# Performance work log

Hardware: AMD Instinct MI355X
Metric: run time of the kernel (lower is better)

## Reference

```python
import jax, jax.numpy as jnp
import numpy as np

N_NODES = 100000


def sage_conv(x, src, dst, Wl, bl, Wr):
    # PyG SAGEConv (aggr='mean'): out = lin_l(mean_{j in N(i)} x_j) + lin_r(x_i)
    msg = x[src]                                                   # [E, d] gather
    agg = jax.ops.segment_sum(msg, dst, num_segments=N_NODES)      # [N, d]
    cnt = jax.ops.segment_sum(jnp.ones((src.shape[0], 1), x.dtype), dst,
                              num_segments=N_NODES)                # [N, 1]
    mean = agg / jnp.maximum(cnt, 1.0)
    return mean @ Wl + bl + x @ Wr


def setup_inputs() -> dict:
    key = jax.random.key(0)
    ks = jax.random.split(key, 9)
    N, E, D_IN = N_NODES, 3200000, 64
    x = jax.random.normal(ks[0], (N, D_IN), dtype=jnp.float32)
    edge_index = jax.random.randint(ks[1], (2, E), 0, N, dtype=jnp.int64)

    def glorot(k, fan_in, fan_out):
        lim = float(np.sqrt(6.0 / (fan_in + fan_out)))
        return jax.random.uniform(k, (fan_in, fan_out), jnp.float32, -lim, lim)

    return {
        "x": x,
        "edge_index": edge_index,
        "W1l": glorot(ks[2], D_IN, 64), "b1": jnp.zeros((64,), jnp.float32),
        "W1r": glorot(ks[3], D_IN, 64),
        "W2l": glorot(ks[4], 64, 32), "b2": jnp.zeros((32,), jnp.float32),
        "W2r": glorot(ks[5], 64, 32),
        "W3l": glorot(ks[6], 32, 1), "b3": jnp.zeros((1,), jnp.float32),
        "W3r": glorot(ks[7], 32, 1),
    }


def reference(x, edge_index, W1l, b1, W1r, W2l, b2, W2r, W3l, b3, W3r):
    src, dst = edge_index[0], edge_index[1]
    h = jax.nn.relu(sage_conv(x, src, dst, W1l, b1, W1r))   # dropout: eval mode (identity)
    h = jax.nn.relu(sage_conv(h, src, dst, W2l, b2, W2r))
    h = sage_conv(h, src, dst, W3l, b3, W3r)
    return jax.nn.sigmoid(h)                                # [N, 1]
```

## Files before the change

kernel.cpp:

```cpp
#include <hip/hip_runtime.h>
#include <math.h>

#define NN 100000
#define NB 391
#define BT 8192
#define CAP 12288

typedef float vfloat2 __attribute__((ext_vector_type(2)));
typedef short short8 __attribute__((ext_vector_type(8)));
typedef float floatx4 __attribute__((ext_vector_type(4)));

__device__ __forceinline__ unsigned short f2bf(float f) {
    unsigned int u = __float_as_uint(f);
    u += 0x7fffu + ((u >> 16) & 1u);
    return (unsigned short)(u >> 16);
}

__device__ __forceinline__ unsigned char f2fp8(float f) {
    const int p = __builtin_amdgcn_cvt_pk_fp8_f32(f, f, 0, false);
    return (unsigned char)(p & 0xFF);
}
template <bool HI>
__device__ __forceinline__ vfloat2 fp8pk2(unsigned int w) {
    return __builtin_amdgcn_cvt_pk_f32_fp8((int)w, HI);
}

template <int D_IN, int CL, int CR, int NPB, int FUSE_IN>
__global__ void __launch_bounds__(256)
mlp_mfma_kernel(const float* __restrict__ in0,
                const float* __restrict__ in1,
                const float* __restrict__ Wl,
                const float* __restrict__ Wr,
                const float* __restrict__ bias,
                unsigned char* __restrict__ yout,
                float* __restrict__ zout,
                int n_nodes) {
    constexpr int COLS = CL + CR;
    constexpr int CT = COLS / 16;
    constexpr int KT = D_IN / 32;
    constexpr int NT = NPB / 16;
    constexpr int KG = D_IN / 8;
    __shared__ short sA[NT * KT * 64 * 8];
    __shared__ short sB[CT * KT * 64 * 8];
    __shared__ float sBias[CR];
    const int t = threadIdx.x;
    const int node0 = blockIdx.x * NPB;

    for (int i = t; i < NPB * KG; i += 256) {
        const int nl = i / KG, kg = i % KG;
        const int n = node0 + nl;
        float v[8];
        if (n < n_nodes) {
            const float4* p = (const float4*)(in0 + (long long)n * D_IN + kg * 8);
            float4 a0 = p[0], a1 = p[1];
            if (FUSE_IN) {
                const float4* q = (const float4*)(in1 + (long long)n * D_IN + kg * 8);
                const float4 b0 = q[0], b1 = q[1];
                a0.x = fmaxf(a0.x + b0.x, 0.f); a0.y = fmaxf(a0.y + b0.y, 0.f);
                a0.z = fmaxf(a0.z + b0.z, 0.f); a0.w = fmaxf(a0.w + b0.w, 0.f);
                a1.x = fmaxf(a1.x + b1.x, 0.f); a1.y = fmaxf(a1.y + b1.y, 0.f);
                a1.z = fmaxf(a1.z + b1.z, 0.f); a1.w = fmaxf(a1.w + b1.w, 0.f);
            }
            v[0] = a0.x; v[1] = a0.y; v[2] = a0.z; v[3] = a0.w;
            v[4] = a1.x; v[5] = a1.y; v[6] = a1.z; v[7] = a1.w;
        } else {
#pragma unroll
            for (int j = 0; j < 8; ++j) v[j] = 0.f;
        }
        short8 s;
#pragma unroll
        for (int j = 0; j < 8; ++j) s[j] = (short)f2bf(v[j]);
        const int nt = nl >> 4, m = nl & 15, kt = kg >> 2, quad = kg & 3;
        ((short8*)sA)[(nt * KT + kt) * 64 + quad * 16 + m] = s;
    }
    for (int i = t; i < CT * KT * 64; i += 256) {
        const int ct = i / (KT * 64);
        const int rem = i % (KT * 64);
        const int kt = rem / 64, L = rem % 64;
        const int c = ct * 16 + (L & 15);
        const int k0 = kt * 32 + (L >> 4) * 8;
        short8 s;
#pragma unroll
        for (int j = 0; j < 8; ++j) {
            const int k = k0 + j;
            const float w = (c < CL) ? Wl[k * CL + c] : Wr[k * CR + (c - CL)];
            s[j] = (short)f2bf(w);
        }
        ((short8*)sB)[i] = s;
    }
    for (int i = t; i < CR; i += 256) sBias[i] = bias[i];
    __syncthreads();

    const int w = t >> 6, lane = t & 63;
    short8 Bf[CT][KT];
#pragma unroll
    for (int ct = 0; ct < CT; ++ct)
#pragma unroll
        for (int kt = 0; kt < KT; ++kt)
            Bf[ct][kt] = ((short8*)sB)[(ct * KT + kt) * 64 + lane];
    const int col = lane & 15, quad = lane >> 4;
#pragma unroll
    for (int nti = 0; nti < NT / 4; ++nti) {
        const int nt = w * (NT / 4) + nti;
        short8 A[KT];
#pragma unroll
        for (int kt = 0; kt < KT; ++kt)
            A[kt] = ((short8*)sA)[(nt * KT + kt) * 64 + lane];
        const int nodeb = node0 + nt * 16 + quad * 4;
#pragma unroll
        for (int ct = 0; ct < CT; ++ct) {
            floatx4 acc = {0.f, 0.f, 0.f, 0.f};
#pragma unroll
            for (int kt = 0; kt < KT; ++kt)
                acc = __builtin_amdgcn_mfma_f32_16x16x32_bf16(A[kt], Bf[ct][kt], acc, 0, 0, 0);
            const int gc = ct * 16 + col;
#pragma unroll
            for (int r = 0; r < 4; ++r) {
                const int node = nodeb + r;
                if (node < n_nodes) {
                    if (gc < CL) {
                        constexpr int CH = CL / 2;
                        const int h = gc / CH;
                        yout[(size_t)h * n_nodes * CH +
                             (long long)node * CH + (gc & (CH - 1))] = f2fp8(acc[r]);
                    } else {
                        zout[(long long)node * CR + (gc - CL)] = acc[r] + sBias[gc - CL];
                    }
                }
            }
        }
    }
}

template <int D_IN>
__global__ void __launch_bounds__(256)
mlp3_kernel(const float* __restrict__ mean,
            const float* __restrict__ z,
            const float* __restrict__ W3l,
            const float* __restrict__ W3r,
            const float* __restrict__ b3,
            float* __restrict__ y,
            float* __restrict__ z3, int n_nodes) {
    __shared__ float swl[D_IN], swr[D_IN];
    const int t = threadIdx.x;
    if (t < D_IN) { swl[t] = W3l[t]; swr[t] = W3r[t]; }
    __syncthreads();
    const int n = blockIdx.x * 256 + t;
    if (n >= n_nodes) return;
    const float4* pm = (const float4*)(mean + (long long)n * D_IN);
    const float4* pz = (const float4*)(z + (long long)n * D_IN);
    float accl = 0.f, accr = 0.f;
#pragma unroll
    for (int q = 0; q < D_IN / 4; ++q) {
        const float4 m4 = pm[q];
        const float4 z4 = pz[q];
        const float h0 = fmaxf(m4.x + z4.x, 0.f);
        const float h1 = fmaxf(m4.y + z4.y, 0.f);
        const float h2 = fmaxf(m4.z + z4.z, 0.f);
        const float h3 = fmaxf(m4.w + z4.w, 0.f);
        accl += h0 * swl[4 * q] + h1 * swl[4 * q + 1] + h2 * swl[4 * q + 2] + h3 * swl[4 * q + 3];
        accr += h0 * swr[4 * q] + h1 * swr[4 * q + 1] + h2 * swr[4 * q + 2] + h3 * swr[4 * q + 3];
    }
    y[n] = accl;
    z3[n] = accr + b3[0];
}

__global__ void bucket_hist_kernel(const int* __restrict__ dst,
                                   int* __restrict__ bcnt, int n_edges) {
    __shared__ int lh[NB];
    for (int i = threadIdx.x; i < NB; i += 256) lh[i] = 0;
    __syncthreads();
    const int stride = gridDim.x * 256;
    for (int i = blockIdx.x * 256 + threadIdx.x; i < n_edges; i += stride)
        atomicAdd(&lh[dst[i] >> 8], 1);
    __syncthreads();
    for (int i = threadIdx.x; i < NB; i += 256)
        if (lh[i]) atomicAdd(&bcnt[i], lh[i]);
}

__global__ void __launch_bounds__(512)
bucket_scan_kernel(const int* __restrict__ bcnt, int* __restrict__ boffs,
                   int* __restrict__ bcursor) {
    __shared__ int s[512];
    const int t = threadIdx.x;
    const int v = (t < NB) ? bcnt[t] : 0;
    s[t] = v;
    __syncthreads();
    for (int off = 1; off < 512; off <<= 1) {
        const int tmp = (t >= off) ? s[t - off] : 0;
        __syncthreads();
        s[t] += tmp;
        __syncthreads();
    }
    const int excl = s[t] - v;
    if (t <= NB) boffs[t] = excl;
    if (t < NB) bcursor[t] = excl;
}

__global__ void __launch_bounds__(512)
bin_edges_kernel(const int* __restrict__ src, const int* __restrict__ dst,
                 int* __restrict__ bcursor, unsigned int* __restrict__ binned,
                 int n_edges) {
    __shared__ unsigned int stage[BT];
    __shared__ unsigned short sbkt[BT];
    __shared__ int lhist[512], lscan[512], lstart[512], gbase[512], lcur[512];
    const int t = threadIdx.x;
    const int e0 = blockIdx.x * BT;
    const int count = min(BT, n_edges - e0);
    lhist[t] = 0;
    __syncthreads();
    for (int i = t; i < count; i += 512) atomicAdd(&lhist[dst[e0 + i] >> 8], 1);
    __syncthreads();
    const int v = lhist[t];
    lscan[t] = v;
    __syncthreads();
    for (int off = 1; off < 512; off <<= 1) {
        const int tmp = (t >= off) ? lscan[t - off] : 0;
        __syncthreads();
        lscan[t] += tmp;
        __syncthreads();
    }
    const int excl = lscan[t] - v;
    lstart[t] = excl;
    lcur[t] = excl;
    if (t < NB && v > 0) gbase[t] = atomicAdd(&bcursor[t], v);
    __syncthreads();
    for (int i = t; i < count; i += 512) {
        const int d = dst[e0 + i];
        const int b = d >> 8;
        const int p = atomicAdd(&lcur[b], 1);
        stage[p] = (unsigned int)src[e0 + i] | ((unsigned int)(d & 255) << 17);
        sbkt[p] = (unsigned short)b;
    }
    __syncthreads();
    for (int i = t; i < count; i += 512) {
        const int b = sbkt[i];
        binned[gbase[b] + (i - lstart[b])] = stage[i];
    }
}

__global__ void __launch_bounds__(1024)
csr_sort_kernel(const unsigned int* __restrict__ binned,
                const int* __restrict__ boffs,
                int* __restrict__ ssrc, int* __restrict__ row_ptr,
                float* __restrict__ inv_deg, int n_nodes, int n_edges) {
    __shared__ int stage[CAP];
    __shared__ int hist[256];
    __shared__ int lexcl[256];
    __shared__ int lcur[256];
    const int t = threadIdx.x;
    const int b = blockIdx.x;
    const int s0 = boffs[b], s1 = boffs[b + 1];
    const int count = s1 - s0;
    if (t < 256) hist[t] = 0;
    __syncthreads();
    for (int i = t; i < count; i += 1024)
        atomicAdd(&hist[binned[s0 + i] >> 17], 1);
    __syncthreads();
    if (t < 256) lexcl[t] = hist[t];
    __syncthreads();
    for (int off = 1; off < 256; off <<= 1) {
        int tmp = 0;
        if (t < 256 && t >= off) tmp = lexcl[t - off];
        __syncthreads();
        if (t < 256) lexcl[t] += tmp;
        __syncthreads();
    }
    if (t < 256) {
        const int excl = lexcl[t] - hist[t];
        lcur[t] = excl;
        const int n = (b << 8) + t;
        if (n < n_nodes) {
            row_ptr[n] = s0 + excl;
            inv_deg[n] = 1.0f / (float)max(hist[t], 1);
        }
    }
    if (b == NB - 1 && t == 0) row_ptr[n_nodes] = n_edges;
    __syncthreads();
    for (int i = t; i < count; i += 1024) {
        const unsigned int v = binned[s0 + i];
        const int p = atomicAdd(&lcur[v >> 17], 1);
        if (p < CAP) stage[p] = (int)(v & 0x1FFFFu);
    }
    __syncthreads();
    for (int i = t; i < count; i += 1024) ssrc[s0 + i] = stage[i];
}

template <int D>
__global__ void __launch_bounds__(256)
agg_mean_fp8_split_kernel(const unsigned int* __restrict__ yb,
                          const int* __restrict__ row_ptr,
                          const int* __restrict__ ssrc,
                          const float* __restrict__ inv_deg,
                          float* __restrict__ mean, int n_nodes) {
    constexpr int CH = D / 2;
    constexpr int G = CH / 16;
    constexpr int NPB = 256 / G;
    const int bid = blockIdx.x;
    const int half = (bid >> 2) & 1;
    const int lb = (bid >> 3) * 4 + (bid & 3);
    const int g = threadIdx.x / G;
    const int lane = threadIdx.x % G;
    const int n = lb * NPB + g;
    if (n >= n_nodes) return;
    const int s0 = row_ptr[n], s1 = row_ptr[n + 1];
    const uint4* yv = (const uint4*)yb + (size_t)half * n_nodes * G;
    float acc[16];
#pragma unroll
    for (int i = 0; i < 16; ++i) acc[i] = 0.f;
    int e = s0;
    for (; e + 4 <= s1; e += 4) {
        int sidx[4];
#pragma unroll
        for (int q = 0; q < 4; ++q) sidx[q] = __builtin_nontemporal_load(ssrc + e + q);
        uint4 v[4];
#pragma unroll
        for (int q = 0; q < 4; ++q) v[q] = yv[(long long)sidx[q] * G + lane];
#pragma unroll
        for (int q = 0; q < 4; ++q) {
            const unsigned int wx = v[q].x, wy = v[q].y, wz = v[q].z, ww = v[q].w;
            vfloat2 p;
            p = fp8pk2<false>(wx); acc[0]  += p.x; acc[1]  += p.y;
            p = fp8pk2<true>(wx);  acc[2]  += p.x; acc[3]  += p.y;
            p = fp8pk2<false>(wy); acc[4]  += p.x; acc[5]  += p.y;
            p = fp8pk2<true>(wy);  acc[6]  += p.x; acc[7]  += p.y;
            p = fp8pk2<false>(wz); acc[8]  += p.x; acc[9]  += p.y;
            p = fp8pk2<true>(wz);  acc[10] += p.x; acc[11] += p.y;
            p = fp8pk2<false>(ww); acc[12] += p.x; acc[13] += p.y;
            p = fp8pk2<true>(ww);  acc[14] += p.x; acc[15] += p.y;
        }
    }
    for (; e < s1; ++e) {
        const int si = __builtin_nontemporal_load(ssrc + e);
        const uint4 v = yv[(long long)si * G + lane];
        vfloat2 p;
        p = fp8pk2<false>(v.x); acc[0]  += p.x; acc[1]  += p.y;
        p = fp8pk2<true>(v.x);  acc[2]  += p.x; acc[3]  += p.y;
        p = fp8pk2<false>(v.y); acc[4]  += p.x; acc[5]  += p.y;
        p = fp8pk2<true>(v.y);  acc[6]  += p.x; acc[7]  += p.y;
        p = fp8pk2<false>(v.z); acc[8]  += p.x; acc[9]  += p.y;
        p = fp8pk2<true>(v.z);  acc[10] += p.x; acc[11] += p.y;
        p = fp8pk2<false>(v.w); acc[12] += p.x; acc[13] += p.y;
        p = fp8pk2<true>(v.w);  acc[14] += p.x; acc[15] += p.y;
    }
    const float inv = inv_deg[n];
    floatx4* mv = (floatx4*)mean + (long long)n * (D / 4) + half * (CH / 4) + lane * 4;
#pragma unroll
    for (int q = 0; q < 4; ++q) {
        floatx4 o = {acc[4 * q] * inv, acc[4 * q + 1] * inv,
                     acc[4 * q + 2] * inv, acc[4 * q + 3] * inv};
        __builtin_nontemporal_store(o, mv + q);
    }
}

__global__ void agg_mean_d1_sig_kernel(const float* __restrict__ y,
                                       const int* __restrict__ row_ptr,
                                       const int* __restrict__ ssrc,
                                       const float* __restrict__ inv_deg,
                                       const float* __restrict__ z3,
                                       float* __restrict__ out, int n_nodes) {
    const int wave = threadIdx.x >> 6;
    const int lane = threadIdx.x & 63;
    const int n = blockIdx.x * 4 + wave;
    if (n >= n_nodes) return;
    const int s0 = row_ptr[n], s1 = row_ptr[n + 1];
    float acc = 0.f;
    for (int e = s0 + lane; e < s1; e += 64)
        acc += y[__builtin_nontemporal_load(ssrc + e)];
    for (int off = 32; off > 0; off >>= 1) acc += __shfl_down(acc, off, 64);
    if (lane == 0) out[n] = 1.0f / (1.0f + expf(-(acc * inv_deg[n] + z3[n])));
}

extern "C" void kernel_launch(void* const* d_in, const int* in_sizes, int n_in,
                              void* d_out, int out_size, void* d_ws, size_t ws_size,
                              hipStream_t stream) {
    const float* x = (const float*)d_in[0];
    const int* edge_index = (const int*)d_in[1];
    const float* W1l = (const float*)d_in[2];
    const float* b1  = (const float*)d_in[3];
    const float* W1r = (const float*)d_in[4];
    const float* W2l = (const float*)d_in[5];
    const float* b2  = (const float*)d_in[6];
    const float* W2r = (const float*)d_in[7];
    const float* W3l = (const float*)d_in[8];
    const float* b3  = (const float*)d_in[9];
    const float* W3r = (const float*)d_in[10];
    float* out = (float*)d_out;

    const int E = in_sizes[1] / 2;
    const int* src = edge_index;
    const int* dst = edge_index + E;

    float* bufY    = (float*)d_ws;
    float* meanB   = bufY + 32LL * NN;
    float* z1      = meanB + 64LL * NN;
    float* z2      = z1 + 64LL * NN;
    float* z3      = z2 + 32LL * NN;
    float* inv_deg = z3 + NN;
    int* bcnt      = (int*)(inv_deg + NN);
    int* boffs     = bcnt + NB;
    int* bcursor   = boffs + NB + 1;
    int* row_ptr   = bcursor + NB;
    int* ssrc      = row_ptr + NN + 1;
    unsigned int* binned = (unsigned int*)z1;

    const int ntiles = (E + BT - 1) / BT;

    (void)hipMemsetAsync(bcnt, 0, NB * sizeof(int), stream);
    bucket_hist_kernel<<<512, 256, 0, stream>>>(dst, bcnt, E);
    bucket_scan_kernel<<<1, 512, 0, stream>>>(bcnt, boffs, bcursor);
    bin_edges_kernel<<<ntiles, 512, 0, stream>>>(src, dst, bcursor, binned, E);
    csr_sort_kernel<<<NB, 1024, 0, stream>>>(binned, boffs, ssrc, row_ptr, inv_deg, NN, E);

    mlp_mfma_kernel<64, 64, 64, 128, 0><<<(NN + 127) / 128, 256, 0, stream>>>(
        x, nullptr, W1l, W1r, b1, (unsigned char*)bufY, z1, NN);
    {
        const int bph = (NN + 127) / 128;
        const int grid = 8 * ((bph + 3) / 4);
        agg_mean_fp8_split_kernel<64><<<grid, 256, 0, stream>>>(
            (const unsigned int*)bufY, row_ptr, ssrc, inv_deg, meanB, NN);
    }

    mlp_mfma_kernel<64, 32, 32, 128, 1><<<(NN + 127) / 128, 256, 0, stream>>>(
        meanB, z1, W2l, W2r, b2, (unsigned char*)bufY, z2, NN);
    {
        const int bph = (NN + 255) / 256;
        const int grid = 8 * ((bph + 3) / 4);
        agg_mean_fp8_split_kernel<32><<<grid, 256, 0, stream>>>(
            (const unsigned int*)bufY, row_ptr, ssrc, inv_deg, meanB, NN);
    }

    mlp3_kernel<32><<<(NN + 255) / 256, 256, 0, stream>>>(
        meanB, z2, W3l, W3r, b3, bufY, z3, NN);
    agg_mean_d1_sig_kernel<<<(NN + 3) / 4, 256, 0, stream>>>(
        bufY, row_ptr, ssrc, inv_deg, z3, out, NN);
}
```

Baseline: 372.6 us.

## Replace feature-split fp8 aggregation with edge-split teams and shuffle reduction

```diff
diff --git a/kernel.cpp b/kernel.cpp
--- a/kernel.cpp
+++ b/kernel.cpp
@@ -118,14 +118,8 @@
             for (int r = 0; r < 4; ++r) {
                 const int node = nodeb + r;
                 if (node < n_nodes) {
-                    if (gc < CL) {
-                        constexpr int CH = CL / 2;
-                        const int h = gc / CH;
-                        yout[(size_t)h * n_nodes * CH +
-                             (long long)node * CH + (gc & (CH - 1))] = f2fp8(acc[r]);
-                    } else {
-                        zout[(long long)node * CR + (gc - CL)] = acc[r] + sBias[gc - CL];
-                    }
+                    if (gc < CL) yout[(long long)node * CL + gc] = f2fp8(acc[r]);
+                    else zout[(long long)node * CR + (gc - CL)] = acc[r] + sBias[gc - CL];
                 }
             }
         }
@@ -286,30 +280,33 @@
     for (int i = t; i < count; i += 1024) ssrc[s0 + i] = stage[i];
 }
 
-template <int D>
+template <int D, int EP>
 __global__ void __launch_bounds__(256)
-agg_mean_fp8_split_kernel(const unsigned int* __restrict__ yb,
-                          const int* __restrict__ row_ptr,
-                          const int* __restrict__ ssrc,
-                          const float* __restrict__ inv_deg,
-                          float* __restrict__ mean, int n_nodes) {
-    constexpr int CH = D / 2;
-    constexpr int G = CH / 16;
-    constexpr int NPB = 256 / G;
-    const int bid = blockIdx.x;
-    const int half = (bid >> 2) & 1;
-    const int lb = (bid >> 3) * 4 + (bid & 3);
-    const int g = threadIdx.x / G;
-    const int lane = threadIdx.x % G;
-    const int n = lb * NPB + g;
+agg_mean_fp8_kernel(const unsigned int* __restrict__ yb,
+                    const int* __restrict__ row_ptr,
+                    const int* __restrict__ ssrc,
+                    const float* __restrict__ inv_deg,
+                    float* __restrict__ mean, int n_nodes) {
+    constexpr int G = D / 16;
+    constexpr int TPN = EP * G;
+    constexpr int NPB = 256 / TPN;
+    const int t = threadIdx.x;
+    const int g = t / TPN;
+    const int sub = t % TPN;
+    const int lane = sub % G;
+    const int team = sub / G;
+    const int n = blockIdx.x * NPB + g;
     if (n >= n_nodes) return;
     const int s0 = row_ptr[n], s1 = row_ptr[n + 1];
-    const uint4* yv = (const uint4*)yb + (size_t)half * n_nodes * G;
+    const int cnt = s1 - s0;
+    const int b0 = s0 + (cnt * team) / EP;
+    const int b1 = s0 + (cnt * (team + 1)) / EP;
+    const uint4* yv = (const uint4*)yb;
     float acc[16];
 #pragma unroll
     for (int i = 0; i < 16; ++i) acc[i] = 0.f;
-    int e = s0;
-    for (; e + 4 <= s1; e += 4) {
+    int e = b0;
+    for (; e + 4 <= b1; e += 4) {
         int sidx[4];
 #pragma unroll
         for (int q = 0; q < 4; ++q) sidx[q] = __builtin_nontemporal_load(ssrc + e + q);
@@ -330,7 +327,7 @@
             p = fp8pk2<true>(ww);  acc[14] += p.x; acc[15] += p.y;
         }
     }
-    for (; e < s1; ++e) {
+    for (; e < b1; ++e) {
         const int si = __builtin_nontemporal_load(ssrc + e);
         const uint4 v = yv[(long long)si * G + lane];
         vfloat2 p;
@@ -343,13 +340,19 @@
         p = fp8pk2<false>(v.w); acc[12] += p.x; acc[13] += p.y;
         p = fp8pk2<true>(v.w);  acc[14] += p.x; acc[15] += p.y;
     }
-    const float inv = inv_deg[n];
-    floatx4* mv = (floatx4*)mean + (long long)n * (D / 4) + half * (CH / 4) + lane * 4;
-#pragma unroll
-    for (int q = 0; q < 4; ++q) {
-        floatx4 o = {acc[4 * q] * inv, acc[4 * q + 1] * inv,
-                     acc[4 * q + 2] * inv, acc[4 * q + 3] * inv};
-        __builtin_nontemporal_store(o, mv + q);
+#pragma unroll
+    for (int o = G; o < TPN; o <<= 1)
+#pragma unroll
+        for (int i = 0; i < 16; ++i) acc[i] += __shfl_xor(acc[i], o, 64);
+    if (team == 0) {
+        const float inv = inv_deg[n];
+        floatx4* mv = (floatx4*)mean + (long long)n * (D / 4) + lane * 4;
+#pragma unroll
+        for (int q = 0; q < 4; ++q) {
+            floatx4 o = {acc[4 * q] * inv, acc[4 * q + 1] * inv,
+                         acc[4 * q + 2] * inv, acc[4 * q + 3] * inv};
+            __builtin_nontemporal_store(o, mv + q);
+        }
     }
 }
 
@@ -414,21 +417,13 @@
 
     mlp_mfma_kernel<64, 64, 64, 128, 0><<<(NN + 127) / 128, 256, 0, stream>>>(
         x, nullptr, W1l, W1r, b1, (unsigned char*)bufY, z1, NN);
-    {
-        const int bph = (NN + 127) / 128;
-        const int grid = 8 * ((bph + 3) / 4);
-        agg_mean_fp8_split_kernel<64><<<grid, 256, 0, stream>>>(
-            (const unsigned int*)bufY, row_ptr, ssrc, inv_deg, meanB, NN);
-    }
+    agg_mean_fp8_kernel<64, 2><<<(NN + 31) / 32, 256, 0, stream>>>(
+        (const unsigned int*)bufY, row_ptr, ssrc, inv_deg, meanB, NN);
 
     mlp_mfma_kernel<64, 32, 32, 128, 1><<<(NN + 127) / 128, 256, 0, stream>>>(
         meanB, z1, W2l, W2r, b2, (unsigned char*)bufY, z2, NN);
-    {
-        const int bph = (NN + 255) / 256;
-        const int grid = 8 * ((bph + 3) / 4);
-        agg_mean_fp8_split_kernel<32><<<grid, 256, 0, stream>>>(
-            (const unsigned int*)bufY, row_ptr, ssrc, inv_deg, meanB, NN);
-    }
+    agg_mean_fp8_kernel<32, 4><<<(NN + 31) / 32, 256, 0, stream>>>(
+        (const unsigned int*)bufY, row_ptr, ssrc, inv_deg, meanB, NN);
 
     mlp3_kernel<32><<<(NN + 255) / 256, 256, 0, stream>>>(
         meanB, z2, W3l, W3r, b3, bufY, z3, NN);
```

Measured after the change: 301.5 us, median of 2. 1.24x faster.
